# Kernel optimization log

Measured on AMD Instinct MI355X. Metric: run time of the kernel, lower is better.

## Reference

```python
import jax, jax.numpy as jnp
import numpy as np

MAX_DISP = 4  # matches init_kwargs


def setup_inputs() -> dict:
    key = jax.random.key(0)
    k1, k2 = jax.random.split(key)
    x_1 = jax.random.normal(k1, (8, 64, 256, 256), dtype=jnp.float32)
    x_2 = jax.random.normal(k2, (8, 64, 256, 256), dtype=jnp.float32)
    return {"x_1": x_1, "x_2": x_2}


def reference(x_1, x_2):
    md = MAX_DISP
    B, C, H, W = x_1.shape
    # zero-pad x_2 spatially by max_disp on all sides
    x2p = jnp.pad(x_2, ((0, 0), (0, 0), (md, md), (md, md)))
    D = 2 * md + 1
    # row-major over (dx, dy), matching torch.meshgrid(indexing='ij')
    outs = [
        jnp.mean(x_1 * jax.lax.dynamic_slice(x2p, (0, 0, dx, dy), (B, C, H, W)),
                 axis=1, keepdims=True)
        for dx in range(D) for dy in range(D)
    ]
    return jnp.concatenate(outs, axis=1)  # [B, D*D, H, W]
```

## Files before the change

### kernel.cpp

```cpp
#include <hip/hip_runtime.h>


namespace {
constexpr int kB = 8;
constexpr int kC = 64;
constexpr int kH = 256;
constexpr int kW = 256;
constexpr int kD = 9;
constexpr int kMD = 4;
constexpr int kChanStride = kH * kW;
}

__global__ __launch_bounds__(64) void corr_kernel(
    const float* __restrict__ x1, const float* __restrict__ x2,
    float* __restrict__ out) {
  const int xcd  = blockIdx.x & 7;
  const int slot = blockIdx.x >> 3;
  const int b  = xcd;
  const int h  = slot / kD;
  const int dx = slot - h * kD;

  const int row = h + dx - kMD;
  const int w0  = (int)threadIdx.x * 4;

  float acc[kD][4];
#pragma unroll
  for (int dy = 0; dy < kD; ++dy)
#pragma unroll
    for (int j = 0; j < 4; ++j) acc[dy][j] = 0.0f;

  if (row >= 0 && row < kH) {
    const float* p1 = x1 + ((size_t)(b * kC) * kH + h) * kW + w0;
    const float* p2 = x2 + ((size_t)(b * kC) * kH + row) * kW + w0;
    const bool hasL = (w0 >= 4);
    const bool hasR = (w0 + 7 < kW);

    float4 a  = *reinterpret_cast<const float4*>(p1);
    float4 tB = *reinterpret_cast<const float4*>(p2);
    float4 tA = make_float4(0.f, 0.f, 0.f, 0.f);
    float4 tC = make_float4(0.f, 0.f, 0.f, 0.f);
    if (hasL) tA = *reinterpret_cast<const float4*>(p2 - 4);
    if (hasR) tC = *reinterpret_cast<const float4*>(p2 + 4);

    for (int c = 0; c < kC; ++c) {
      float4 na = a, nA = tA, nB = tB, nC = tC;
      if (c + 1 < kC) {
        p1 += kChanStride;
        p2 += kChanStride;
        na = *reinterpret_cast<const float4*>(p1);
        nB = *reinterpret_cast<const float4*>(p2);
        nA = make_float4(0.f, 0.f, 0.f, 0.f);
        nC = make_float4(0.f, 0.f, 0.f, 0.f);
        if (hasL) nA = *reinterpret_cast<const float4*>(p2 - 4);
        if (hasR) nC = *reinterpret_cast<const float4*>(p2 + 4);
      }

      const float av[4] = {a.x, a.y, a.z, a.w};
      const float t[12] = {tA.x, tA.y, tA.z, tA.w,
                           tB.x, tB.y, tB.z, tB.w,
                           tC.x, tC.y, tC.z, tC.w};
#pragma unroll
      for (int dy = 0; dy < kD; ++dy)
#pragma unroll
        for (int j = 0; j < 4; ++j)
          acc[dy][j] = fmaf(av[j], t[dy + j], acc[dy][j]);

      a = na; tA = nA; tB = nB; tC = nC;
    }
  }

  const float inv = 1.0f / (float)kC;
  float* po = out + (((size_t)b * (kD * kD) + dx * kD) * kH + h) * kW + w0;
#pragma unroll
  for (int dy = 0; dy < kD; ++dy) {
    float4 o = make_float4(acc[dy][0] * inv, acc[dy][1] * inv,
                           acc[dy][2] * inv, acc[dy][3] * inv);
    *reinterpret_cast<float4*>(po) = o;
    po += (size_t)kH * kW;
  }
}

extern "C" void kernel_launch(void* const* d_in, const int* in_sizes, int n_in,
                              void* d_out, int out_size, void* d_ws, size_t ws_size,
                              hipStream_t stream) {
  const float* x1 = (const float*)d_in[0];
  const float* x2 = (const float*)d_in[1];
  float* out = (float*)d_out;
  const int grid = kB * kH * kD;
  corr_kernel<<<grid, 64, 0, stream>>>(x1, x2, out);
}
```

Before: 216.0 us.

## Compute 8 columns per thread and two rows per block

Each thread now computes 8 output columns instead of 4, and each 64-thread block covers two image rows, so the grid is halved. This raises the ratio of FMAs to loads, since 16 loaded x2 values serve 72 FMAs instead of 12 serving 36. Boundary-row handling becomes per-lane predication rather than skipping the whole block. The cost is roughly double the accumulator registers, which may lower occupancy, and fewer blocks in flight.

```diff
diff --git a/kernel.cpp b/kernel.cpp
--- a/kernel.cpp
+++ b/kernel.cpp
@@ -17,65 +17,84 @@
   const int xcd  = blockIdx.x & 7;
   const int slot = blockIdx.x >> 3;
   const int b  = xcd;
-  const int h  = slot / kD;
-  const int dx = slot - h * kD;
+  const int hp = slot / kD;
+  const int dx = slot - hp * kD;
 
-  const int row = h + dx - kMD;
-  const int w0  = (int)threadIdx.x * 4;
+  const int lane = (int)threadIdx.x;
+  const int half = lane >> 5;
+  const int lh   = lane & 31;
+  const int h    = hp * 2 + half;
+  const int row  = h + dx - kMD;
+  const int w0   = lh * 8;
 
-  float acc[kD][4];
+  const bool rowok = (row >= 0) && (row < kH);
+  const bool hasL  = rowok && (lh > 0);
+  const bool hasR  = rowok && (lh < 31);
+
+  float acc[kD][8];
 #pragma unroll
   for (int dy = 0; dy < kD; ++dy)
 #pragma unroll
-    for (int j = 0; j < 4; ++j) acc[dy][j] = 0.0f;
+    for (int j = 0; j < 8; ++j) acc[dy][j] = 0.0f;
 
-  if (row >= 0 && row < kH) {
-    const float* p1 = x1 + ((size_t)(b * kC) * kH + h) * kW + w0;
-    const float* p2 = x2 + ((size_t)(b * kC) * kH + row) * kW + w0;
-    const bool hasL = (w0 >= 4);
-    const bool hasR = (w0 + 7 < kW);
+  const float* p1 = x1 + ((size_t)(b * kC) * kH + h) * kW + w0;
+  const float* p2 = x2 + ((size_t)(b * kC) * kH + row) * kW + w0;
 
-    float4 a  = *reinterpret_cast<const float4*>(p1);
-    float4 tB = *reinterpret_cast<const float4*>(p2);
-    float4 tA = make_float4(0.f, 0.f, 0.f, 0.f);
-    float4 tC = make_float4(0.f, 0.f, 0.f, 0.f);
-    if (hasL) tA = *reinterpret_cast<const float4*>(p2 - 4);
-    if (hasR) tC = *reinterpret_cast<const float4*>(p2 + 4);
+  const float4 z = make_float4(0.f, 0.f, 0.f, 0.f);
 
-    for (int c = 0; c < kC; ++c) {
-      float4 na = a, nA = tA, nB = tB, nC = tC;
-      if (c + 1 < kC) {
-        p1 += kChanStride;
-        p2 += kChanStride;
-        na = *reinterpret_cast<const float4*>(p1);
-        nB = *reinterpret_cast<const float4*>(p2);
-        nA = make_float4(0.f, 0.f, 0.f, 0.f);
-        nC = make_float4(0.f, 0.f, 0.f, 0.f);
-        if (hasL) nA = *reinterpret_cast<const float4*>(p2 - 4);
-        if (hasR) nC = *reinterpret_cast<const float4*>(p2 + 4);
-      }
+  float4 a0, a1, t0, t1, t2, t3;
+  a0 = *reinterpret_cast<const float4*>(p1);
+  a1 = *reinterpret_cast<const float4*>(p1 + 4);
+  t0 = hasL  ? *reinterpret_cast<const float4*>(p2 - 4) : z;
+  t1 = rowok ? *reinterpret_cast<const float4*>(p2)     : z;
+  t2 = rowok ? *reinterpret_cast<const float4*>(p2 + 4) : z;
+  t3 = hasR  ? *reinterpret_cast<const float4*>(p2 + 8) : z;
 
-      const float av[4] = {a.x, a.y, a.z, a.w};
-      const float t[12] = {tA.x, tA.y, tA.z, tA.w,
-                           tB.x, tB.y, tB.z, tB.w,
-                           tC.x, tC.y, tC.z, tC.w};
+#pragma unroll 2
+  for (int c = 0; c < kC - 1; ++c) {
+    p1 += kChanStride;
+    p2 += kChanStride;
+    float4 na0 = *reinterpret_cast<const float4*>(p1);
+    float4 na1 = *reinterpret_cast<const float4*>(p1 + 4);
+    float4 nt0 = hasL  ? *reinterpret_cast<const float4*>(p2 - 4) : z;
+    float4 nt1 = rowok ? *reinterpret_cast<const float4*>(p2)     : z;
+    float4 nt2 = rowok ? *reinterpret_cast<const float4*>(p2 + 4) : z;
+    float4 nt3 = hasR  ? *reinterpret_cast<const float4*>(p2 + 8) : z;
+
+    {
+      const float av[8] = {a0.x, a0.y, a0.z, a0.w, a1.x, a1.y, a1.z, a1.w};
+      const float t[16] = {t0.x, t0.y, t0.z, t0.w, t1.x, t1.y, t1.z, t1.w,
+                           t2.x, t2.y, t2.z, t2.w, t3.x, t3.y, t3.z, t3.w};
 #pragma unroll
       for (int dy = 0; dy < kD; ++dy)
 #pragma unroll
-        for (int j = 0; j < 4; ++j)
+        for (int j = 0; j < 8; ++j)
           acc[dy][j] = fmaf(av[j], t[dy + j], acc[dy][j]);
+    }
 
-      a = na; tA = nA; tB = nB; tC = nC;
-    }
+    a0 = na0; a1 = na1; t0 = nt0; t1 = nt1; t2 = nt2; t3 = nt3;
+  }
+  {
+    const float av[8] = {a0.x, a0.y, a0.z, a0.w, a1.x, a1.y, a1.z, a1.w};
+    const float t[16] = {t0.x, t0.y, t0.z, t0.w, t1.x, t1.y, t1.z, t1.w,
+                         t2.x, t2.y, t2.z, t2.w, t3.x, t3.y, t3.z, t3.w};
+#pragma unroll
+    for (int dy = 0; dy < kD; ++dy)
+#pragma unroll
+      for (int j = 0; j < 8; ++j)
+        acc[dy][j] = fmaf(av[j], t[dy + j], acc[dy][j]);
   }
 
   const float inv = 1.0f / (float)kC;
   float* po = out + (((size_t)b * (kD * kD) + dx * kD) * kH + h) * kW + w0;
 #pragma unroll
   for (int dy = 0; dy < kD; ++dy) {
-    float4 o = make_float4(acc[dy][0] * inv, acc[dy][1] * inv,
-                           acc[dy][2] * inv, acc[dy][3] * inv);
-    *reinterpret_cast<float4*>(po) = o;
+    float4 o0 = make_float4(acc[dy][0] * inv, acc[dy][1] * inv,
+                            acc[dy][2] * inv, acc[dy][3] * inv);
+    float4 o1 = make_float4(acc[dy][4] * inv, acc[dy][5] * inv,
+                            acc[dy][6] * inv, acc[dy][7] * inv);
+    *reinterpret_cast<float4*>(po)     = o0;
+    *reinterpret_cast<float4*>(po + 4) = o1;
     po += (size_t)kH * kW;
   }
 }
@@ -86,6 +105,6 @@
   const float* x1 = (const float*)d_in[0];
   const float* x2 = (const float*)d_in[1];
   float* out = (float*)d_out;
-  const int grid = kB * kH * kD;
+  const int grid = kB * (kH / 2) * kD;
   corr_kernel<<<grid, 64, 0, stream>>>(x1, x2, out);
 }
```

New measurement: 232.9 us. +7.8%, slower.
